# Performance work log

Measured on AMD Instinct MI355X. Metric: run time of the kernel, lower is better.

## Reference

```python
import jax, jax.numpy as jnp
import numpy as np

HEADS = 8
BN_EPS = 1e-5

def _bn(x2d, g, b):
    # torch BatchNorm1d in training mode: biased batch stats
    mu = x2d.mean(0)
    var = x2d.var(0)
    return (x2d - mu) * jax.lax.rsqrt(var + BN_EPS) * g + b

def _window_indices(H):
    # exclusive-end box coordinates, in the exact order of the torch loop
    m = H // 2
    r0, r1, c0, c1 = [], [], [], []
    for i in range(1, m + 1):
        wins = [(m - i, m + i + 1, m - i, m + i + 1),  # full square
                (m - i, m + 1,     m - i, m + i + 1),  # top half
                (m,     m + i + 1, m - i, m + i + 1),  # bottom half
                (m - i, m + i + 1, m - i, m + 1),      # left half
                (m - i, m + i + 1, m,     m + i + 1)]  # right half
        for a, b, c, d in wins:
            r0.append(a); r1.append(b); c0.append(c); c1.append(d)
    r0 = np.array(r0); r1 = np.array(r1); c0 = np.array(c0); c1 = np.array(c1)
    counts = ((r1 - r0) * (c1 - c0)).astype(np.float32)
    return r0, r1, c0, c1, counts

def _box_sums(P, r0, r1, c0, c1):
    # P: padded 2D prefix sum [B, C, H+1, H+1]; returns [B, C, K]
    return P[:, :, r1, c1] - P[:, :, r0, c1] - P[:, :, r1, c0] + P[:, :, r0, c0]

def _integral(img):
    return jnp.pad(jnp.cumsum(jnp.cumsum(img, axis=2), axis=3), ((0, 0), (0, 0), (1, 0), (1, 0)))

def setup_inputs() -> dict:
    key = jax.random.key(0)
    ks = jax.random.split(key, 8)
    B, Cin, H = 64, 512, 31
    C = 512  # heads * base_dim
    x = jax.random.normal(ks[0], (B, Cin, H, H), dtype=jnp.float32)
    w_v = jax.random.normal(ks[1], (Cin, C), dtype=jnp.float32) * 0.02
    w_k = jax.random.normal(ks[2], (Cin, C), dtype=jnp.float32) * 0.02
    w_fc = jax.random.normal(ks[3], (Cin + C, 512), dtype=jnp.float32) * 0.02
    z = lambda n: jnp.zeros((n,), jnp.float32)
    o = lambda n: jnp.ones((n,), jnp.float32)
    return {"x": x,
            "w_v": w_v, "b_v": z(C), "g_vn": o(C), "b_vn": z(C),
            "w_k": w_k, "b_k": z(C), "g_kn": o(C), "b_kn": z(C),
            "w_fc": w_fc, "b_fc": z(512), "g_fcn": o(512), "b_fcn": z(512)}

def reference(x, w_v, b_v, g_vn, b_vn, w_k, b_k, g_kn, b_kn, w_fc, b_fc, g_fcn, b_fcn):
    B, Cin, H, W = x.shape
    N = H * W
    C = w_v.shape[1]
    d = C // HEADS
    m = H // 2
    xt = x.reshape(B, Cin, N).transpose(0, 2, 1)       # [B, N, Cin]
    x0 = xt[:, N // 2, :]                              # [B, Cin] center pixel feature
    flat = xt.reshape(B * N, Cin)
    v = jax.nn.relu(_bn(flat @ w_v + b_v, g_vn, b_vn))
    v = v.reshape(B, N, C).transpose(0, 2, 1).reshape(B, C, H, H)
    k = _bn(flat @ w_k + b_k, g_kn, b_kn).reshape(B, N, HEADS, d).transpose(0, 2, 1, 3)  # [B,h,N,d]
    q = k[:, :, N // 2, :]                             # [B, h, d]
    attn = jax.nn.softmax(jnp.einsum('bhd,bhnd->bhn', q, k) * (d ** -0.5), axis=-1)      # [B,h,N]
    attn_full = jnp.broadcast_to(attn[:, :, None, :], (B, HEADS, d, N)).reshape(B, C, H, H)
    xw = attn_full * v                                 # attn-weighted values [B,C,H,H]
    eps = 1e-16
    r0, r1, c0, c1, counts = _window_indices(H)
    Px = _integral(xw)
    Pa = _integral(attn_full)
    mx = _box_sums(Px, r0, r1, c0, c1) / counts        # window means of xw   [B,C,K]
    ma = _box_sums(Pa, r0, r1, c0, c1) / counts        # window means of attn [B,C,K]
    y_win = (mx / (ma + eps)).transpose(0, 2, 1)       # [B, K, C]
    y = jnp.concatenate([xw[:, :, m, m][:, None, :], y_win], axis=1)  # [B, n, C]
    # F.normalize(p=2, dim=2)
    y = y / jnp.maximum(jnp.linalg.norm(y, axis=2, keepdims=True), 1e-12)
    n = y.shape[1]
    yy = jnp.concatenate([jnp.broadcast_to(x0[:, None, :], (B, n, Cin)), y], axis=-1)
    out = jax.nn.relu(_bn(yy.reshape(B * n, Cin + C) @ w_fc + b_fc, g_fcn, b_fcn))
    return out.reshape(B, n, -1)
```

## Files before the change

### kernel.cpp

```cpp
#include <hip/hip_runtime.h>
#include <stdint.h>

#define DEV __device__ __forceinline__

typedef __bf16 bf16x8 __attribute__((ext_vector_type(8)));
typedef unsigned short u16x8 __attribute__((ext_vector_type(8)));
typedef float f32x4 __attribute__((ext_vector_type(4)));

#define NS 992

DEV uint16_t f2bf(float f) {
    union { float f; uint32_t u; } v; v.f = f;
    uint32_t r = v.u + 0x7fffu + ((v.u >> 16) & 1u);
    return (uint16_t)(r >> 16);
}
DEV float bf2f(uint16_t h) {
    union { uint32_t u; float f; } v; v.u = ((uint32_t)h) << 16;
    return v.f;
}
DEV float bflo(uint32_t w) { union { uint32_t u; float f; } v; v.u = w << 16; return v.f; }
DEV float bfhi(uint32_t w) { union { uint32_t u; float f; } v; v.u = w & 0xffff0000u; return v.f; }

#if __has_builtin(__builtin_amdgcn_cvt_pk_bf16_f32)
typedef __bf16 bf16x2 __attribute__((ext_vector_type(2)));
DEV uint32_t pk2bf(float lo, float hi) {
    bf16x2 r = __builtin_amdgcn_cvt_pk_bf16_f32(lo, hi);
    return __builtin_bit_cast(uint32_t, r);
}
#else
DEV uint32_t pk2bf(float lo, float hi) {
    return (uint32_t)f2bf(lo) | ((uint32_t)f2bf(hi) << 16);
}
#endif

DEV float scan32(float v, int lane) {
    #pragma unroll
    for (int d = 1; d < 32; d <<= 1) {
        float o = __shfl_up(v, d, 32);
        if (lane >= d) v += o;
    }
    return v;
}

DEV void win_idx(int w, int& r0, int& r1, int& c0, int& c1) {
    int i = w / 5 + 1, t = w % 5;
    const int m = 15;
    switch (t) {
        case 0: r0 = m - i; r1 = m + i + 1; c0 = m - i; c1 = m + i + 1; break;
        case 1: r0 = m - i; r1 = m + 1;     c0 = m - i; c1 = m + i + 1; break;
        case 2: r0 = m;     r1 = m + i + 1; c0 = m - i; c1 = m + i + 1; break;
        case 3: r0 = m - i; r1 = m + i + 1; c0 = m - i; c1 = m + 1;     break;
        default:r0 = m - i; r1 = m + i + 1; c0 = m;     c1 = m + i + 1; break;
    }
}

#if __has_builtin(__builtin_amdgcn_global_load_lds)
DEV void async16(const uint16_t* g, uint16_t* l) {
    __builtin_amdgcn_global_load_lds(
        (const __attribute__((address_space(1))) uint32_t*)g,
        (__attribute__((address_space(3))) uint32_t*)l, 16, 0, 0);
}
#else
DEV void async16(const uint16_t* g, uint16_t* l) {
    *(u16x8*)l = *(const u16x8*)g;
}
#endif

__global__ void k_convert_x(const float* __restrict__ x, uint16_t* __restrict__ xbt) {
    __shared__ float tile[32][33];
    int b = blockIdx.z;
    int n0 = blockIdx.x * 32;
    int c0 = blockIdx.y * 32;
    int tx = threadIdx.x, ty = threadIdx.y;
    #pragma unroll
    for (int i = 0; i < 4; ++i) {
        int c = c0 + ty + 8 * i;
        int n = n0 + tx;
        float v = 0.f;
        if (n < 961) v = x[((size_t)b * 512 + c) * 961 + n];
        tile[ty + 8 * i][tx] = v;
    }
    __syncthreads();
    int idx = ty * 32 + tx;
    int c4 = (idx & 7) * 4;
    int nl = idx >> 3;
    int n = n0 + nl;
    ushort4 val;
    val.x = f2bf(tile[c4 + 0][nl]);
    val.y = f2bf(tile[c4 + 1][nl]);
    val.z = f2bf(tile[c4 + 2][nl]);
    val.w = f2bf(tile[c4 + 3][nl]);
    *(ushort4*)&xbt[((size_t)b * NS + n) * 512 + c0 + c4] = val;
}

__global__ void k_convert_w(const float* __restrict__ wv, const float* __restrict__ wk,
                            const float* __restrict__ wfc,
                            uint16_t* __restrict__ wvkt, uint16_t* __restrict__ wfct) {
    int idx = blockIdx.x * 256 + threadIdx.x;
    if (idx < 524288) {
        int j = idx >> 9, k = idx & 511;
        float v = (j < 512) ? wv[(size_t)k * 512 + j] : wk[(size_t)k * 512 + (j - 512)];
        wvkt[idx] = f2bf(v);
    } else {
        int t = idx - 524288;
        int j = t >> 10, k = t & 1023;
        wfct[t] = f2bf(wfc[(size_t)k * 512 + j]);
    }
}

template<int K, int EPI>
__global__ __launch_bounds__(256, 4)
void k_gemm(const uint16_t* __restrict__ A, const uint16_t* __restrict__ Bt,
            uint16_t* __restrict__ out_v, uint16_t* __restrict__ out_k,
            float* __restrict__ out_f,
            float* __restrict__ colsum, float* __restrict__ colsq)
{
    __shared__ __align__(16) uint16_t sbuf[16384];
    __shared__ float sStat[256];
    uint16_t* sA0 = sbuf;
    uint16_t* sA1 = sbuf + 4096;
    uint16_t* sB0 = sbuf + 8192;
    uint16_t* sB1 = sbuf + 12288;

    const int tid = threadIdx.x;
    const int wave = tid >> 6, lane = tid & 63;
    const int quad = lane >> 4, l16 = lane & 15;
    int m0, j0;
    if constexpr (EPI == 0) {
        int lin = blockIdx.x;
        int xcd = lin & 7, rest = lin >> 3;
        int jb = rest & 7, mhi = rest >> 3;
        m0 = (mhi * 8 + xcd) * 128; j0 = jb * 128;
    } else {
        m0 = blockIdx.y * 128; j0 = blockIdx.x * 128;
    }
    const int wm = wave >> 1, wj = wave & 1;

    const f32x4 fzero = {0.f, 0.f, 0.f, 0.f};
    f32x4 acc[4][4];
    #pragma unroll
    for (int i = 0; i < 4; ++i)
        #pragma unroll
        for (int j = 0; j < 4; ++j) acc[i][j] = fzero;

    const int c0 = tid;
    const int mA0 = c0 >> 2, kq0 = c0 & 3;
    const int c1 = tid + 256;
    const int mA1 = c1 >> 2, kq1 = c1 & 3;

    const int KT = K / 64;
    for (int kt = 0; kt < KT; ++kt) {
        const uint16_t* Ak = A + (size_t)m0 * K + kt * 64;
        const uint16_t* Bk = Bt + (size_t)j0 * K + kt * 64;
        async16(Ak + (size_t)mA0 * K + kq0 * 8,      &sA0[c0 * 8]);
        async16(Ak + (size_t)mA1 * K + kq1 * 8,      &sA0[c1 * 8]);
        async16(Ak + (size_t)mA0 * K + 32 + kq0 * 8, &sA1[c0 * 8]);
        async16(Ak + (size_t)mA1 * K + 32 + kq1 * 8, &sA1[c1 * 8]);
        async16(Bk + (size_t)mA0 * K + kq0 * 8,      &sB0[c0 * 8]);
        async16(Bk + (size_t)mA1 * K + kq1 * 8,      &sB0[c1 * 8]);
        async16(Bk + (size_t)mA0 * K + 32 + kq0 * 8, &sB1[c0 * 8]);
        async16(Bk + (size_t)mA1 * K + 32 + kq1 * 8, &sB1[c1 * 8]);
        __syncthreads();
        #pragma unroll
        for (int p = 0; p < 2; ++p) {
            const uint16_t* pA = p ? sA1 : sA0;
            const uint16_t* pB = p ? sB1 : sB0;
            bf16x8 af[4], bfr[4];
            #pragma unroll
            for (int i = 0; i < 4; ++i) {
                int m = wm * 64 + i * 16 + l16;
                u16x8 r = *(const u16x8*)&pA[m * 32 + quad * 8];
                af[i] = __builtin_bit_cast(bf16x8, r);
            }
            #pragma unroll
            for (int j = 0; j < 4; ++j) {
                int jj = wj * 64 + j * 16 + l16;
                u16x8 r = *(const u16x8*)&pB[jj * 32 + quad * 8];
                bfr[j] = __builtin_bit_cast(bf16x8, r);
            }
            #pragma unroll
            for (int i = 0; i < 4; ++i)
                #pragma unroll
                for (int j = 0; j < 4; ++j)
                    acc[i][j] = __builtin_amdgcn_mfma_f32_16x16x32_bf16(af[i], bfr[j], acc[i][j], 0, 0, 0);
        }
        __syncthreads();
    }

    sStat[tid] = 0.f;
    __syncthreads();

    #pragma unroll
    for (int j = 0; j < 4; ++j) {
        const int col_local = wj * 64 + j * 16 + l16;
        float ls = 0.f, lq = 0.f;
        #pragma unroll
        for (int i = 0; i < 4; ++i) {
            #pragma unroll
            for (int reg = 0; reg < 4; ++reg) {
                const float val = acc[i][j][reg];
                ls += val; lq += val * val;
                if constexpr (EPI == 1) {
                    const int r = m0 + wm * 64 + i * 16 + quad * 4 + reg;
                    out_f[(size_t)r * 512 + (j0 + col_local)] = val;
                }
            }
        }
        ls += __shfl_xor(ls, 16); lq += __shfl_xor(lq, 16);
        ls += __shfl_xor(ls, 32); lq += __shfl_xor(lq, 32);
        if (quad == 0) {
            atomicAdd(&sStat[col_local], ls);
            atomicAdd(&sStat[128 + col_local], lq);
        }
    }
    __syncthreads();
    if (tid < 128) atomicAdd(&colsum[j0 + tid], sStat[tid]);
    else           atomicAdd(&colsq[j0 + (tid & 127)], sStat[tid]);

    if constexpr (EPI == 0) {
        #pragma unroll
        for (int ch = 0; ch < 2; ++ch) {
            if (wj == ch) {
                #pragma unroll
                for (int j = 0; j < 4; ++j) {
                    const int c = j * 16 + l16;
                    #pragma unroll
                    for (int i = 0; i < 4; ++i) {
                        const int rloc = wm * 64 + i * 16 + quad * 4;
                        uint2 pp;
                        pp.x = pk2bf(acc[i][j][0], acc[i][j][1]);
                        pp.y = pk2bf(acc[i][j][2], acc[i][j][3]);
                        *(uint2*)&sbuf[c * 136 + rloc] = pp;
                    }
                }
            }
            __syncthreads();
            const int jg = j0 + ch * 64;
            uint16_t* const outp = (jg < 512) ? out_v : out_k;
            const int jbase = (jg < 512) ? jg : jg - 512;
            #pragma unroll
            for (int s = 0; s < 8; ++s) {
                const int chunk = tid + 256 * s;
                const int c = chunk >> 5, q = chunk & 31;
                uint2 val = *(const uint2*)&sbuf[c * 136 + q * 4];
                const int r = m0 + q * 4;
                const unsigned bb_ = (unsigned)r / (unsigned)NS;
                const unsigned nn = (unsigned)r - bb_ * (unsigned)NS;
                *(uint2*)&outp[((size_t)bb_ * 512 + jbase + c) * NS + nn] = val;
            }
            __syncthreads();
        }
    }
}

__global__ __launch_bounds__(1024, 2)
void k_attnwin(const uint16_t* __restrict__ kraw, const uint16_t* __restrict__ vraw,
               const float* __restrict__ colsum, const float* __restrict__ colsq,
               const float* __restrict__ g_kn, const float* __restrict__ b_kn,
               const float* __restrict__ g_vn, const float* __restrict__ b_vn,
               float* __restrict__ y)
{
    __shared__ float qa[64];
    __shared__ float va[64], vb[64];
    __shared__ float atv[964];
    __shared__ float xw[4][964];
    __shared__ float maw_s[76];
    __shared__ float red[16];
    __shared__ float s_qb, s_bmax, s_inv;

    const int bh = blockIdx.x;
    const int b = bh >> 3, h = bh & 7;
    const int tid = threadIdx.x;
    constexpr float invM = 1.f / 61504.f;

    if (tid < 64) {
        int c = h * 64 + tid;
        float mean = colsum[512 + c] * invM;
        float q_ = colsq[512 + c] * invM;
        float a = g_kn[c] * rsqrtf(q_ - mean * mean + 1e-5f);
        float bb = b_kn[c] - mean * a;
        float kr = bf2f(kraw[((size_t)b * 512 + c) * NS + 480]);
        float qv = kr * a + bb;
        qa[tid] = qv * a;
        float qb = qv * bb;
        #pragma unroll
        for (int off = 32; off; off >>= 1) qb += __shfl_down(qb, off);
        if (tid == 0) s_qb = qb;
    } else if (tid >= 64 && tid < 128) {
        int t = tid - 64;
        int c = h * 64 + t;
        float mean = colsum[c] * invM;
        float q_ = colsq[c] * invM;
        float a = g_vn[c] * rsqrtf(q_ - mean * mean + 1e-5f);
        va[t] = a;
        vb[t] = b_vn[c] - mean * a;
    }
    __syncthreads();

    float lg = -1e30f;
    if (tid < 961) {
        const uint16_t* kp = kraw + ((size_t)b * 512 + h * 64) * NS + tid;
        float acc = 0.f;
        #pragma unroll 16
        for (int dd = 0; dd < 64; ++dd)
            acc += qa[dd] * bf2f(kp[(size_t)dd * NS]);
        lg = (acc + s_qb) * 0.125f;
    }
    float lmax = lg;
    #pragma unroll
    for (int off = 32; off; off >>= 1) lmax = fmaxf(lmax, __shfl_xor(lmax, off));
    if ((tid & 63) == 0) red[tid >> 6] = lmax;
    __syncthreads();
    if (tid < 64) {
        float v = (tid < 16) ? red[tid] : -1e30f;
        #pragma unroll
        for (int off = 8; off; off >>= 1) v = fmaxf(v, __shfl_xor(v, off));
        if (tid == 0) s_bmax = v;
    }
    __syncthreads();
    float e = (tid < 961) ? __expf(lg - s_bmax) : 0.f;
    float lsum = e;
    #pragma unroll
    for (int off = 32; off; off >>= 1) lsum += __shfl_xor(lsum, off);
    if ((tid & 63) == 0) red[tid >> 6] = lsum;
    __syncthreads();
    if (tid < 64) {
        float v = (tid < 16) ? red[tid] : 0.f;
        #pragma unroll
        for (int off = 8; off; off >>= 1) v += __shfl_xor(v, off);
        if (tid == 0) s_inv = 1.f / v;
    }
    __syncthreads();
    if (tid < 961) {
        float a = e * s_inv;
        atv[tid] = a;
        xw[0][tid] = a;
    }
    __syncthreads();

    {
        int row = tid >> 5, col = tid & 31;
        bool on = (tid < 992) && (col < 31);
        float v = on ? xw[0][row * 31 + col] : 0.f;
        v = scan32(v, col);
        if (on) xw[0][row * 31 + col] = v;
    }
    __syncthreads();
    {
        int cc = tid >> 5, r = tid & 31;
        bool on = (tid < 992) && (r < 31);
        float v = on ? xw[0][r * 31 + cc] : 0.f;
        v = scan32(v, r);
        if (on) xw[0][r * 31 + cc] = v;
    }
    __syncthreads();
    if (tid < 75) {
        int r0, r1, c0, c1;
        win_idx(tid, r0, r1, c0, c1);
        auto S = [&](int r, int c) -> float { return (r < 0 || c < 0) ? 0.f : xw[0][r * 31 + c]; };
        float box = S(r1 - 1, c1 - 1) - S(r0 - 1, c1 - 1) - S(r1 - 1, c0 - 1) + S(r0 - 1, c0 - 1);
        float cnt = (float)((r1 - r0) * (c1 - c0));
        maw_s[tid] = box / cnt;
    }
    __syncthreads();

    const uint16_t* vbase = vraw + ((size_t)b * 512 + h * 64) * NS + tid;
    float pv[4];
    if (tid < 961) {
        #pragma unroll
        for (int u = 0; u < 4; ++u) pv[u] = bf2f(vbase[(size_t)u * NS]);
    }
    for (int cp = 0; cp < 16; ++cp) {
        if (tid < 961) {
            float myatt = atv[tid];
            #pragma unroll
            for (int u = 0; u < 4; ++u) {
                int cl = cp * 4 + u;
                float w = fmaxf(pv[u] * va[cl] + vb[cl], 0.f) * myatt;
                xw[u][tid] = w;
                if (tid == 480) y[(size_t)b * 76 * 512 + (h * 64 + cl)] = w;
            }
            if (cp < 15) {
                #pragma unroll
                for (int u = 0; u < 4; ++u) pv[u] = bf2f(vbase[(size_t)(cp * 4 + 4 + u) * NS]);
            }
        }
        __syncthreads();
        {
            int row = tid >> 5, col = tid & 31;
            bool on = (tid < 992) && (col < 31);
            #pragma unroll
            for (int u = 0; u < 4; ++u) {
                float v = on ? xw[u][row * 31 + col] : 0.f;
                v = scan32(v, col);
                if (on) xw[u][row * 31 + col] = v;
            }
        }
        __syncthreads();
        {
            int cc = tid >> 5, r = tid & 31;
            bool on = (tid < 992) && (r < 31);
            #pragma unroll
            for (int u = 0; u < 4; ++u) {
                float v = on ? xw[u][r * 31 + cc] : 0.f;
                v = scan32(v, r);
                if (on) xw[u][r * 31 + cc] = v;
            }
        }
        __syncthreads();
        {
            int u = tid >> 8, w = tid & 255;
            if (w < 75) {
                int r0, r1, c0, c1;
                win_idx(w, r0, r1, c0, c1);
                auto S = [&](int r, int c) -> float { return (r < 0 || c < 0) ? 0.f : xw[u][r * 31 + c]; };
                float box = S(r1 - 1, c1 - 1) - S(r0 - 1, c1 - 1) - S(r1 - 1, c0 - 1) + S(r0 - 1, c0 - 1);
                float cnt = (float)((r1 - r0) * (c1 - c0));
                float mx = box / cnt;
                int cl = cp * 4 + u;
                y[((size_t)b * 76 + 1 + w) * 512 + (h * 64 + cl)] = mx / (maw_s[w] + 1e-16f);
            }
        }
        __syncthreads();
    }
}

__global__ void k_build_yy(const float* __restrict__ y, const uint16_t* __restrict__ xbt,
                           uint16_t* __restrict__ yy)
{
    __shared__ float red[4];
    int row = blockIdx.x;
    int b = row / 76;
    int tid = threadIdx.x;
    const float* yp = y + (size_t)row * 512;
    float v0 = yp[tid], v1 = yp[tid + 256];
    float ss = v0 * v0 + v1 * v1;
    for (int off = 32; off; off >>= 1) ss += __shfl_xor(ss, off);
    if ((tid & 63) == 0) red[tid >> 6] = ss;
    __syncthreads();
    float tot = red[0] + red[1] + red[2] + red[3];
    float inv = 1.f / fmaxf(sqrtf(tot), 1e-12f);
    uint16_t* op = yy + (size_t)row * 1024;
    const uint16_t* x0p = xbt + ((size_t)b * NS + 480) * 512;
    op[tid]           = x0p[tid];
    op[tid + 256]     = x0p[tid + 256];
    op[512 + tid]       = f2bf(v0 * inv);
    op[512 + tid + 256] = f2bf(v1 * inv);
}

__global__ void k_fcout(const float* __restrict__ fcraw,
                        const float* __restrict__ colsum, const float* __restrict__ colsq,
                        const float* __restrict__ g, const float* __restrict__ be,
                        float* __restrict__ out)
{
    size_t idx = (size_t)blockIdx.x * 256 + threadIdx.x;
    if (idx < (size_t)4864 * 512) {
        int j = (int)(idx & 511);
        constexpr float invM = 1.f / 4864.f;
        float mean = colsum[j] * invM;
        float q_ = colsq[j] * invM;
        float a = g[j] * rsqrtf(q_ - mean * mean + 1e-5f);
        float bb = be[j] - mean * a;
        out[idx] = fmaxf(fcraw[idx] * a + bb, 0.f);
    }
}

extern "C" void kernel_launch(void* const* d_in, const int* in_sizes, int n_in,
                              void* d_out, int out_size, void* d_ws, size_t ws_size,
                              hipStream_t stream)
{
    (void)in_sizes; (void)n_in; (void)out_size; (void)ws_size;
    const float* x    = (const float*)d_in[0];
    const float* w_v  = (const float*)d_in[1];
    const float* g_vn = (const float*)d_in[3];
    const float* b_vn = (const float*)d_in[4];
    const float* w_k  = (const float*)d_in[5];
    const float* g_kn = (const float*)d_in[7];
    const float* b_kn = (const float*)d_in[8];
    const float* w_fc = (const float*)d_in[9];
    const float* g_fcn = (const float*)d_in[11];
    const float* b_fcn = (const float*)d_in[12];
    float* out = (float*)d_out;

    char* base = (char*)d_ws;
    size_t off = 0;
    auto alloc = [&](size_t bytes) -> void* {
        void* p = base + off;
        off += (bytes + 255) & ~(size_t)255;
        return p;
    };
    uint16_t* xbt  = (uint16_t*)alloc((size_t)64 * NS * 512 * 2);
    uint16_t* wvkt = (uint16_t*)alloc((size_t)1024 * 512 * 2);
    uint16_t* wfct = (uint16_t*)alloc((size_t)512 * 1024 * 2);
    uint16_t* vraw = (uint16_t*)alloc((size_t)64 * 512 * NS * 2);
    uint16_t* kraw = (uint16_t*)alloc((size_t)64 * 512 * NS * 2);
    float* stats   = (float*)alloc(3072 * 4);
    float* y       = (float*)alloc((size_t)64 * 76 * 512 * 4);
    uint16_t* yy   = (uint16_t*)alloc((size_t)4864 * 1024 * 2);
    float* fcraw   = (float*)alloc((size_t)4864 * 512 * 4);

    hipMemsetAsync(stats, 0, 3072 * 4, stream);
    k_convert_x<<<dim3(31, 16, 64), dim3(32, 8), 0, stream>>>(x, xbt);
    k_convert_w<<<4096, 256, 0, stream>>>(w_v, w_k, w_fc, wvkt, wfct);

    k_gemm<512, 0><<<3968, 256, 0, stream>>>(xbt, wvkt, vraw, kraw, nullptr,
                                             stats, stats + 1024);

    k_attnwin<<<512, 1024, 0, stream>>>(kraw, vraw, stats, stats + 1024,
                                        g_kn, b_kn, g_vn, b_vn, y);
    k_build_yy<<<4864, 256, 0, stream>>>(y, xbt, yy);

    k_gemm<1024, 1><<<dim3(4, 38), 256, 0, stream>>>(yy, wfct, nullptr, nullptr, fcraw,
                                                     stats + 2048, stats + 2560);
    k_fcout<<<9728, 256, 0, stream>>>(fcraw, stats + 2048, stats + 2560, g_fcn, b_fcn, out);
}
```

Measured before the change: 462.7 us.

## Compute window box sums via MFMA with a precomputed window mask matrix

Replaces the per-channel 2D prefix-scan window sums in the attention/window kernel with a bf16 MFMA product between a precomputed 0/1 window-membership matrix (75 windows × 961 positions) and the attention-weighted values. The kernel moves from 1024 to 256 threads per block, and the logits pass now handles four positions per thread with vector loads. The spatial stride NS is padded to 1024 so the GEMM epilogue indexes with shifts and rows are aligned. Window sums are now accumulated from bf16-rounded products, which costs some precision, and the padding adds a little memory traffic and GEMM work.

```diff
diff --git a/kernel.cpp b/kernel.cpp
--- a/kernel.cpp
+++ b/kernel.cpp
@@ -5,9 +5,10 @@
 
 typedef __bf16 bf16x8 __attribute__((ext_vector_type(8)));
 typedef unsigned short u16x8 __attribute__((ext_vector_type(8)));
+typedef uint32_t u32x4 __attribute__((ext_vector_type(4)));
 typedef float f32x4 __attribute__((ext_vector_type(4)));
 
-#define NS 992
+#define NS 1024
 
 DEV uint16_t f2bf(float f) {
     union { float f; uint32_t u; } v; v.f = f;
@@ -18,8 +19,6 @@
     union { uint32_t u; float f; } v; v.u = ((uint32_t)h) << 16;
     return v.f;
 }
-DEV float bflo(uint32_t w) { union { uint32_t u; float f; } v; v.u = w << 16; return v.f; }
-DEV float bfhi(uint32_t w) { union { uint32_t u; float f; } v; v.u = w & 0xffff0000u; return v.f; }
 
 #if __has_builtin(__builtin_amdgcn_cvt_pk_bf16_f32)
 typedef __bf16 bf16x2 __attribute__((ext_vector_type(2)));
@@ -95,16 +94,33 @@
 
 __global__ void k_convert_w(const float* __restrict__ wv, const float* __restrict__ wk,
                             const float* __restrict__ wfc,
-                            uint16_t* __restrict__ wvkt, uint16_t* __restrict__ wfct) {
+                            uint16_t* __restrict__ wvkt, uint16_t* __restrict__ wfct,
+                            uint16_t* __restrict__ wfrag) {
     int idx = blockIdx.x * 256 + threadIdx.x;
     if (idx < 524288) {
         int j = idx >> 9, k = idx & 511;
         float v = (j < 512) ? wv[(size_t)k * 512 + j] : wk[(size_t)k * 512 + (j - 512)];
         wvkt[idx] = f2bf(v);
-    } else {
+    } else if (idx < 1048576) {
         int t = idx - 524288;
         int j = t >> 10, k = t & 1023;
         wfct[t] = f2bf(wfc[(size_t)k * 512 + j]);
+    } else {
+        int t = idx - 1048576;
+        int e = t & 7;
+        int lane = (t >> 3) & 63;
+        int kt = (t >> 9) & 31;
+        int mt = t >> 14;
+        int m = mt * 16 + (lane & 15);
+        int k = kt * 32 + (lane >> 4) * 8 + e;
+        uint16_t out = 0;
+        if (m < 75 && k < 961) {
+            int r = k / 31, cc = k - r * 31;
+            int r0, r1, c0, c1;
+            win_idx(m, r0, r1, c0, c1);
+            if (r >= r0 && r < r1 && cc >= c0 && cc < c1) out = 0x3f80;
+        }
+        wfrag[t] = out;
     }
 }
 
@@ -244,8 +260,8 @@
                 const int c = chunk >> 5, q = chunk & 31;
                 uint2 val = *(const uint2*)&sbuf[c * 136 + q * 4];
                 const int r = m0 + q * 4;
-                const unsigned bb_ = (unsigned)r / (unsigned)NS;
-                const unsigned nn = (unsigned)r - bb_ * (unsigned)NS;
+                const unsigned bb_ = (unsigned)r >> 10;
+                const unsigned nn = (unsigned)r & 1023u;
                 *(uint2*)&outp[((size_t)bb_ * 512 + jbase + c) * NS + nn] = val;
             }
             __syncthreads();
@@ -253,8 +269,9 @@
     }
 }
 
-__global__ __launch_bounds__(1024, 2)
+__global__ __launch_bounds__(256, 4)
 void k_attnwin(const uint16_t* __restrict__ kraw, const uint16_t* __restrict__ vraw,
+               const uint16_t* __restrict__ wfrag,
                const float* __restrict__ colsum, const float* __restrict__ colsq,
                const float* __restrict__ g_kn, const float* __restrict__ b_kn,
                const float* __restrict__ g_vn, const float* __restrict__ b_vn,
@@ -262,15 +279,18 @@
 {
     __shared__ float qa[64];
     __shared__ float va[64], vb[64];
-    __shared__ float atv[964];
-    __shared__ float xw[4][964];
-    __shared__ float maw_s[76];
-    __shared__ float red[16];
+    __shared__ float atv[992];
+    __shared__ __align__(16) uint16_t attb[1024];
+    __shared__ float maw_s[80];
+    __shared__ float cnt_s[80];
+    __shared__ float red[4];
     __shared__ float s_qb, s_bmax, s_inv;
 
     const int bh = blockIdx.x;
     const int b = bh >> 3, h = bh & 7;
     const int tid = threadIdx.x;
+    const int lane = tid & 63, wave = tid >> 6;
+    const int quad = lane >> 4, l16 = lane & 15;
     constexpr float invM = 1.f / 61504.f;
 
     if (tid < 64) {
@@ -286,7 +306,7 @@
         #pragma unroll
         for (int off = 32; off; off >>= 1) qb += __shfl_down(qb, off);
         if (tid == 0) s_qb = qb;
-    } else if (tid >= 64 && tid < 128) {
+    } else if (tid < 128) {
         int t = tid - 64;
         int c = h * 64 + t;
         float mean = colsum[c] * invM;
@@ -297,131 +317,148 @@
     }
     __syncthreads();
 
-    float lg = -1e30f;
-    if (tid < 961) {
-        const uint16_t* kp = kraw + ((size_t)b * 512 + h * 64) * NS + tid;
-        float acc = 0.f;
-        #pragma unroll 16
-        for (int dd = 0; dd < 64; ++dd)
-            acc += qa[dd] * bf2f(kp[(size_t)dd * NS]);
-        lg = (acc + s_qb) * 0.125f;
-    }
-    float lmax = lg;
+    const int n4 = tid * 4;
+    float lg[4];
+    float lmax = -1e30f;
+    {
+        const uint16_t* kp = kraw + ((size_t)b * 512 + h * 64) * NS + n4;
+        float a0 = 0.f, a1 = 0.f, a2 = 0.f, a3 = 0.f;
+        if (n4 < 961) {
+            #pragma unroll 16
+            for (int dd = 0; dd < 64; ++dd) {
+                uint2 kk = *(const uint2*)(kp + (size_t)dd * NS);
+                u16x8 kk4 = {};
+                kk4[0] = (uint16_t)(kk.x & 0xffffu);
+                kk4[1] = (uint16_t)(kk.x >> 16);
+                kk4[2] = (uint16_t)(kk.y & 0xffffu);
+                kk4[3] = (uint16_t)(kk.y >> 16);
+                float q = qa[dd];
+                a0 += q * bf2f(kk4[0]);
+                a1 += q * bf2f(kk4[1]);
+                a2 += q * bf2f(kk4[2]);
+                a3 += q * bf2f(kk4[3]);
+            }
+        }
+        lg[0] = a0; lg[1] = a1; lg[2] = a2; lg[3] = a3;
+        #pragma unroll
+        for (int i = 0; i < 4; ++i) {
+            lg[i] = (lg[i] + s_qb) * 0.125f;
+            if (n4 + i < 961) lmax = fmaxf(lmax, lg[i]);
+        }
+    }
     #pragma unroll
     for (int off = 32; off; off >>= 1) lmax = fmaxf(lmax, __shfl_xor(lmax, off));
-    if ((tid & 63) == 0) red[tid >> 6] = lmax;
-    __syncthreads();
+    if (lane == 0) red[wave] = lmax;
+    __syncthreads();
+    if (tid == 0) s_bmax = fmaxf(fmaxf(red[0], red[1]), fmaxf(red[2], red[3]));
+    __syncthreads();
+    float lsum = 0.f;
+    #pragma unroll
+    for (int i = 0; i < 4; ++i) {
+        float e = (n4 + i < 961) ? __expf(lg[i] - s_bmax) : 0.f;
+        lg[i] = e;
+        lsum += e;
+    }
+    #pragma unroll
+    for (int off = 32; off; off >>= 1) lsum += __shfl_xor(lsum, off);
+    if (lane == 0) red[wave] = lsum;
+    __syncthreads();
+    if (tid == 0) s_inv = 1.f / (red[0] + red[1] + red[2] + red[3]);
+    __syncthreads();
+    {
+        uint2 pk;
+        float w0 = (n4 + 0 < 961) ? lg[0] * s_inv : 0.f;
+        float w1 = (n4 + 1 < 961) ? lg[1] * s_inv : 0.f;
+        float w2 = (n4 + 2 < 961) ? lg[2] * s_inv : 0.f;
+        float w3 = (n4 + 3 < 961) ? lg[3] * s_inv : 0.f;
+        pk.x = pk2bf(w0, w1);
+        pk.y = pk2bf(w2, w3);
+        *(uint2*)&attb[n4] = pk;
+        #pragma unroll
+        for (int i = 0; i < 4; ++i)
+            if (n4 + i < 961) atv[n4 + i] = lg[i] * s_inv;
+    }
+    __syncthreads();
+
     if (tid < 64) {
-        float v = (tid < 16) ? red[tid] : -1e30f;
-        #pragma unroll
-        for (int off = 8; off; off >>= 1) v = fmaxf(v, __shfl_xor(v, off));
-        if (tid == 0) s_bmax = v;
-    }
-    __syncthreads();
-    float e = (tid < 961) ? __expf(lg - s_bmax) : 0.f;
-    float lsum = e;
-    #pragma unroll
-    for (int off = 32; off; off >>= 1) lsum += __shfl_xor(lsum, off);
-    if ((tid & 63) == 0) red[tid >> 6] = lsum;
-    __syncthreads();
-    if (tid < 64) {
-        float v = (tid < 16) ? red[tid] : 0.f;
-        #pragma unroll
-        for (int off = 8; off; off >>= 1) v += __shfl_xor(v, off);
-        if (tid == 0) s_inv = 1.f / v;
-    }
-    __syncthreads();
-    if (tid < 961) {
-        float a = e * s_inv;
-        atv[tid] = a;
-        xw[0][tid] = a;
+        float vv = bf2f(vraw[((size_t)(b * 512 + h * 64 + tid)) * NS + 480]);
+        y[(size_t)b * 76 * 512 + h * 64 + tid] = fmaxf(vv * va[tid] + vb[tid], 0.f) * atv[480];
     }
     __syncthreads();
 
     {
-        int row = tid >> 5, col = tid & 31;
-        bool on = (tid < 992) && (col < 31);
-        float v = on ? xw[0][row * 31 + col] : 0.f;
-        v = scan32(v, col);
-        if (on) xw[0][row * 31 + col] = v;
+        int col = tid & 31, r8 = tid >> 5;
+        #pragma unroll
+        for (int p = 0; p < 4; ++p) {
+            int row = p * 8 + r8;
+            bool on = (row < 31) && (col < 31);
+            float v = on ? atv[row * 31 + col] : 0.f;
+            v = scan32(v, col);
+            if (on) atv[row * 31 + col] = v;
+        }
     }
     __syncthreads();
     {
-        int cc = tid >> 5, r = tid & 31;
-        bool on = (tid < 992) && (r < 31);
-        float v = on ? xw[0][r * 31 + cc] : 0.f;
-        v = scan32(v, r);
-        if (on) xw[0][r * 31 + cc] = v;
+        int r = tid & 31, c8 = tid >> 5;
+        #pragma unroll
+        for (int p = 0; p < 4; ++p) {
+            int cc = p * 8 + c8;
+            bool on = (cc < 31) && (r < 31);
+            float v = on ? atv[r * 31 + cc] : 0.f;
+            v = scan32(v, r);
+            if (on) atv[r * 31 + cc] = v;
+        }
     }
     __syncthreads();
     if (tid < 75) {
         int r0, r1, c0, c1;
         win_idx(tid, r0, r1, c0, c1);
-        auto S = [&](int r, int c) -> float { return (r < 0 || c < 0) ? 0.f : xw[0][r * 31 + c]; };
+        auto S = [&](int r, int c) -> float { return (r < 0 || c < 0) ? 0.f : atv[r * 31 + c]; };
         float box = S(r1 - 1, c1 - 1) - S(r0 - 1, c1 - 1) - S(r1 - 1, c0 - 1) + S(r0 - 1, c0 - 1);
         float cnt = (float)((r1 - r0) * (c1 - c0));
+        cnt_s[tid] = cnt;
         maw_s[tid] = box / cnt;
     }
     __syncthreads();
 
-    const uint16_t* vbase = vraw + ((size_t)b * 512 + h * 64) * NS + tid;
-    float pv[4];
-    if (tid < 961) {
-        #pragma unroll
-        for (int u = 0; u < 4; ++u) pv[u] = bf2f(vbase[(size_t)u * NS]);
-    }
-    for (int cp = 0; cp < 16; ++cp) {
-        if (tid < 961) {
-            float myatt = atv[tid];
-            #pragma unroll
-            for (int u = 0; u < 4; ++u) {
-                int cl = cp * 4 + u;
-                float w = fmaxf(pv[u] * va[cl] + vb[cl], 0.f) * myatt;
-                xw[u][tid] = w;
-                if (tid == 480) y[(size_t)b * 76 * 512 + (h * 64 + cl)] = w;
-            }
-            if (cp < 15) {
-                #pragma unroll
-                for (int u = 0; u < 4; ++u) pv[u] = bf2f(vbase[(size_t)(cp * 4 + 4 + u) * NS]);
-            }
-        }
-        __syncthreads();
-        {
-            int row = tid >> 5, col = tid & 31;
-            bool on = (tid < 992) && (col < 31);
-            #pragma unroll
-            for (int u = 0; u < 4; ++u) {
-                float v = on ? xw[u][row * 31 + col] : 0.f;
-                v = scan32(v, col);
-                if (on) xw[u][row * 31 + col] = v;
-            }
-        }
-        __syncthreads();
-        {
-            int cc = tid >> 5, r = tid & 31;
-            bool on = (tid < 992) && (r < 31);
-            #pragma unroll
-            for (int u = 0; u < 4; ++u) {
-                float v = on ? xw[u][r * 31 + cc] : 0.f;
-                v = scan32(v, r);
-                if (on) xw[u][r * 31 + cc] = v;
-            }
-        }
-        __syncthreads();
-        {
-            int u = tid >> 8, w = tid & 255;
-            if (w < 75) {
-                int r0, r1, c0, c1;
-                win_idx(w, r0, r1, c0, c1);
-                auto S = [&](int r, int c) -> float { return (r < 0 || c < 0) ? 0.f : xw[u][r * 31 + c]; };
-                float box = S(r1 - 1, c1 - 1) - S(r0 - 1, c1 - 1) - S(r1 - 1, c0 - 1) + S(r0 - 1, c0 - 1);
-                float cnt = (float)((r1 - r0) * (c1 - c0));
-                float mx = box / cnt;
-                int cl = cp * 4 + u;
-                y[((size_t)b * 76 + 1 + w) * 512 + (h * 64 + cl)] = mx / (maw_s[w] + 1e-16f);
-            }
-        }
-        __syncthreads();
+    {
+        const int cl = wave * 16 + l16;
+        const float a_bn = va[cl], b_bn = vb[cl];
+        const uint16_t* vp = vraw + ((size_t)(b * 512 + h * 64 + cl)) * NS + quad * 8;
+        f32x4 acc5[5];
+        const f32x4 fz = {0.f, 0.f, 0.f, 0.f};
+        #pragma unroll
+        for (int mt = 0; mt < 5; ++mt) acc5[mt] = fz;
+        for (int kt = 0; kt < 31; ++kt) {
+            u16x8 vv = *(const u16x8*)(vp + kt * 32);
+            u16x8 aa = *(const u16x8*)&attb[kt * 32 + quad * 8];
+            u32x4 bwu;
+            #pragma unroll
+            for (int e = 0; e < 4; ++e) {
+                float x0 = fmaxf(bf2f(vv[2 * e]) * a_bn + b_bn, 0.f) * bf2f(aa[2 * e]);
+                float x1 = fmaxf(bf2f(vv[2 * e + 1]) * a_bn + b_bn, 0.f) * bf2f(aa[2 * e + 1]);
+                bwu[e] = pk2bf(x0, x1);
+            }
+            bf16x8 bfr = __builtin_bit_cast(bf16x8, bwu);
+            #pragma unroll
+            for (int mt = 0; mt < 5; ++mt) {
+                u16x8 wf = *(const u16x8*)&wfrag[(((mt * 32 + kt) * 64 + lane)) * 8];
+                acc5[mt] = __builtin_amdgcn_mfma_f32_16x16x32_bf16(
+                    __builtin_bit_cast(bf16x8, wf), bfr, acc5[mt], 0, 0, 0);
+            }
+        }
+        const int cg = h * 64 + cl;
+        #pragma unroll
+        for (int mt = 0; mt < 5; ++mt) {
+            #pragma unroll
+            for (int reg = 0; reg < 4; ++reg) {
+                int w = mt * 16 + quad * 4 + reg;
+                if (w < 75) {
+                    float mx = acc5[mt][reg] / cnt_s[w];
+                    y[((size_t)b * 76 + 1 + w) * 512 + cg] = mx / (maw_s[w] + 1e-16f);
+                }
+            }
+        }
     }
 }
 
@@ -492,6 +529,7 @@
     uint16_t* xbt  = (uint16_t*)alloc((size_t)64 * NS * 512 * 2);
     uint16_t* wvkt = (uint16_t*)alloc((size_t)1024 * 512 * 2);
     uint16_t* wfct = (uint16_t*)alloc((size_t)512 * 1024 * 2);
+    uint16_t* wfrag = (uint16_t*)alloc((size_t)5 * 32 * 64 * 8 * 2);
     uint16_t* vraw = (uint16_t*)alloc((size_t)64 * 512 * NS * 2);
     uint16_t* kraw = (uint16_t*)alloc((size_t)64 * 512 * NS * 2);
     float* stats   = (float*)alloc(3072 * 4);
@@ -500,14 +538,14 @@
     float* fcraw   = (float*)alloc((size_t)4864 * 512 * 4);
 
     hipMemsetAsync(stats, 0, 3072 * 4, stream);
-    k_convert_x<<<dim3(31, 16, 64), dim3(32, 8), 0, stream>>>(x, xbt);
-    k_convert_w<<<4096, 256, 0, stream>>>(w_v, w_k, w_fc, wvkt, wfct);
-
-    k_gemm<512, 0><<<3968, 256, 0, stream>>>(xbt, wvkt, vraw, kraw, nullptr,
+    k_convert_x<<<dim3(32, 16, 64), dim3(32, 8), 0, stream>>>(x, xbt);
+    k_convert_w<<<4416, 256, 0, stream>>>(w_v, w_k, w_fc, wvkt, wfct, wfrag);
+
+    k_gemm<512, 0><<<4096, 256, 0, stream>>>(xbt, wvkt, vraw, kraw, nullptr,
                                              stats, stats + 1024);
 
-    k_attnwin<<<512, 1024, 0, stream>>>(kraw, vraw, stats, stats + 1024,
-                                        g_kn, b_kn, g_vn, b_vn, y);
+    k_attnwin<<<512, 256, 0, stream>>>(kraw, vraw, wfrag, stats, stats + 1024,
+                                       g_kn, b_kn, g_vn, b_vn, y);
     k_build_yy<<<4864, 256, 0, stream>>>(y, xbt, yy);
 
     k_gemm<1024, 1><<<dim3(4, 38), 256, 0, stream>>>(yy, wfct, nullptr, nullptr, fcraw,
```

Measured after the change: 423.6 us. 8.5% less time.
